# Performance work log

Measured on AMD Instinct MI355X. Metric: run time of the kernel, lower is better.

The kernel has to match this reference:

```python
import math
import jax, jax.numpy as jnp
import numpy as np

B, S, D, H = 4, 2048, 512, 8
DH = D // H
NUM_BUCKETS = 32
MAX_DISTANCE = 128


def _relative_position_bucket(rel_pos, num_buckets=NUM_BUCKETS, max_distance=MAX_DISTANCE):
    # bidirectional T5 bucketing (faithful to the torch staticmethod)
    num_buckets = num_buckets // 2
    rel_buckets = (rel_pos > 0).astype(jnp.int32) * num_buckets
    rel_pos = jnp.abs(rel_pos)
    max_exact = num_buckets // 2
    is_small = rel_pos < max_exact
    # clamp log arg to >=1 element to avoid -inf cast (masked out by is_small anyway)
    rp_f = jnp.maximum(rel_pos, 1).astype(jnp.float32)
    large = max_exact + (
        jnp.log(rp_f / max_exact) / math.log(max_distance / max_exact) * (num_buckets - max_exact)
    ).astype(jnp.int32)
    large = jnp.minimum(large, num_buckets - 1)
    return rel_buckets + jnp.where(is_small, rel_pos, large)


def setup_inputs() -> dict:
    rng = jax.random.key(0)
    ks = jax.random.split(rng, 12)
    s = 0.02
    return {
        'key':   jax.random.normal(ks[0], (B, S, D), jnp.float32),
        'value': jax.random.normal(ks[1], (B, S, D), jnp.float32),
        'query': jax.random.normal(ks[2], (B, S, D), jnp.float32),
        'Wq': jax.random.normal(ks[3], (D, D), jnp.float32) * s,
        'bq': jnp.zeros((D,), jnp.float32),
        'Wk': jax.random.normal(ks[4], (D, D), jnp.float32) * s,
        'bk': jnp.zeros((D,), jnp.float32),
        'Wv': jax.random.normal(ks[5], (D, D), jnp.float32) * s,
        'bv': jnp.zeros((D,), jnp.float32),
        'Wo': jax.random.normal(ks[6], (D, D), jnp.float32) * s,
        'bo': jnp.zeros((D,), jnp.float32),
        'rel_bias': jax.random.normal(ks[7], (NUM_BUCKETS, H), jnp.float32) * s,
        'mask': jax.random.bernoulli(ks[8], 0.5, (B, S, S)),
    }


def reference(key, value, query, Wq, bq, Wk, bk, Wv, bv, Wo, bo, rel_bias, mask):
    def shape(x):  # [B,S,D] -> [B,H,S,DH]
        return x.reshape(B, -1, H, DH).transpose(0, 2, 1, 3)

    q = shape(query @ Wq + bq) / math.sqrt(DH)
    k = shape(key @ Wk + bk)
    v = shape(value @ Wv + bv)

    scores = jnp.einsum('bhqd,bhkd->bhqk', q, k)  # [B,H,S,S]

    # T5 relative position bias
    rel_pos = jnp.arange(S)[None, :] - jnp.arange(S)[:, None]  # [S,S] memory - query
    buckets = _relative_position_bucket(rel_pos)
    pos_bias = rel_bias[buckets]                     # [S,S,H]
    scores = scores + pos_bias.transpose(2, 0, 1)[None]  # [1,H,S,S]

    scores = jnp.where(mask[:, None, :, :], jnp.float32(-1e18), scores)
    attn = jax.nn.softmax(scores, axis=-1)  # dropout p=0 -> identity

    ctx = jnp.einsum('bhqk,bhkd->bhqd', attn, v)
    ctx = ctx.transpose(0, 2, 1, 3).reshape(B, -1, D)
    return ctx @ Wo + bo
```

## Files before the change

kernel.cpp:

```cpp
#include <hip/hip_runtime.h>
#include <hip/hip_bf16.h>
#include <math.h>

#define BB 4
#define SS 2048
#define DD 512
#define HH 8
#define DHH 64
#define KPAD 72
#define GPAD 72
#define LOG2E 1.44269504088896340736f

typedef __attribute__((ext_vector_type(8))) short short8;
typedef __attribute__((ext_vector_type(4))) float f32x4;
typedef __attribute__((ext_vector_type(16))) float f32x16;
typedef __attribute__((ext_vector_type(4))) unsigned short ushort4v;
typedef unsigned short ushort;
typedef unsigned char uchar;
typedef unsigned int u32;
typedef unsigned long long u64;

static __device__ __forceinline__ ushort f2b(float x) {
    __hip_bfloat16 h = __float2bfloat16(x);
    return *reinterpret_cast<ushort*>(&h);
}

__global__ __launch_bounds__(256) void pack_mask_kernel(const void* __restrict__ mask,
                                                        u64* __restrict__ mwords) {
    __shared__ int sflag;
    const int tid = threadIdx.x;
    if (tid == 0) sflag = 0;
    __syncthreads();
    u32 probe = ((const u32*)mask)[tid];
    if (__any(probe > 1u) && (tid & 63) == 0) sflag = 1;
    __syncthreads();
    const bool bytemode = sflag != 0;

    int idx = blockIdx.x * 256 + tid;
    int w = idx & 31;
    int row = idx >> 5;
    u64 bits = 0ull;
    if (bytemode) {
        const uint4* p4 = (const uint4*)((const uchar*)mask + (size_t)row * SS + w * 64);
#pragma unroll
        for (int i = 0; i < 4; ++i) {
            uint4 v = p4[i];
            unsigned int a[4] = {v.x, v.y, v.z, v.w};
#pragma unroll
            for (int j = 0; j < 4; ++j)
#pragma unroll
                for (int byte = 0; byte < 4; ++byte)
                    if ((a[j] >> (byte * 8)) & 0xffu) bits |= 1ull << (i * 16 + j * 4 + byte);
        }
    } else {
        const int4* p4 = (const int4*)((const int*)mask + (size_t)row * SS + w * 64);
#pragma unroll
        for (int i = 0; i < 16; ++i) {
            int4 v = p4[i];
            if (v.x) bits |= 1ull << (i * 4 + 0);
            if (v.y) bits |= 1ull << (i * 4 + 1);
            if (v.z) bits |= 1ull << (i * 4 + 2);
            if (v.w) bits |= 1ull << (i * 4 + 3);
        }
    }
    mwords[idx] = bits;
}

__device__ __forceinline__ int t5_bucket(int rel) {
    int rb = (rel > 0) ? 16 : 0;
    int ap = rel < 0 ? -rel : rel;
    if (ap < 8) return rb + ap;
    float t = logf((float)ap * 0.125f) / 2.77258872985839844f * 8.0f;
    int large = 8 + (int)t;
    if (large > 15) large = 15;
    return rb + large;
}

__global__ __launch_bounds__(256) void bias_table_kernel(const float* __restrict__ rel_bias,
                                                         float* __restrict__ tbl) {
    int i = blockIdx.x * 256 + threadIdx.x;
    int h = i >> 12;
    int d = (i & 4095) - 2047;
    tbl[i] = LOG2E * rel_bias[t5_bucket(d) * HH + h];
}

__global__ __launch_bounds__(256) void wtrans_kernel(const float* __restrict__ W0, const float* __restrict__ W1,
                                                     const float* __restrict__ W2, const float* __restrict__ W3,
                                                     ushort* __restrict__ T0, ushort* __restrict__ T1,
                                                     ushort* __restrict__ T2, ushort* __restrict__ T3) {
    __shared__ float tile[64][65];
    const float* W = blockIdx.z == 0 ? W0 : blockIdx.z == 1 ? W1 : blockIdx.z == 2 ? W2 : W3;
    ushort*     T = blockIdx.z == 0 ? T0 : blockIdx.z == 1 ? T1 : blockIdx.z == 2 ? T2 : T3;
    const int n0 = blockIdx.x * 64, k0 = blockIdx.y * 64;
    const int tr = threadIdx.x >> 4, tc = threadIdx.x & 15;
#pragma unroll
    for (int i = 0; i < 4; ++i) {
        int r = i * 16 + tr;
        float4 v = *(const float4*)&W[(size_t)(k0 + r) * 512 + n0 + tc * 4];
        tile[r][tc * 4 + 0] = v.x; tile[r][tc * 4 + 1] = v.y;
        tile[r][tc * 4 + 2] = v.z; tile[r][tc * 4 + 3] = v.w;
    }
    __syncthreads();
#pragma unroll
    for (int i = 0; i < 4; ++i) {
        int rn = i * 16 + tr;
        ushort4v o;
#pragma unroll
        for (int j = 0; j < 4; ++j) o[j] = f2b(tile[tc * 4 + j][rn]);
        *(ushort4v*)&T[(size_t)(n0 + rn) * 512 + k0 + tc * 4] = o;
    }
}

__global__ __launch_bounds__(256) void qkv_gemm(const float* __restrict__ Xq, const float* __restrict__ Xk,
                                                const float* __restrict__ Xv,
                                                const ushort* __restrict__ Wqt, const ushort* __restrict__ Wkt,
                                                const ushort* __restrict__ Wvt,
                                                const float* __restrict__ bqp, const float* __restrict__ bkp,
                                                const float* __restrict__ bvp,
                                                ushort* __restrict__ Yq, ushort* __restrict__ Yk,
                                                ushort* __restrict__ Yv) {
    __shared__ ushort Als[128 * GPAD];
    __shared__ ushort Bls[128 * GPAD];
    const int z = blockIdx.z;
    const float* A    = z == 0 ? Xq : z == 1 ? Xk : Xv;
    const ushort* Bt  = z == 0 ? Wqt : z == 1 ? Wkt : Wvt;
    const float* bias = z == 0 ? bqp : z == 1 ? bkp : bvp;
    const float scale = z == 0 ? 0.125f * LOG2E : 1.0f;

    const int tid = threadIdx.x;
    const int lane = tid & 63;
    const int wid = tid >> 6;
    const int lq = lane & 15, lg = lane >> 4;
    const int wr = wid >> 1, wc = wid & 1;
    const int bm = blockIdx.x * 128;
    const int bn = blockIdx.y * 128;

    f32x4 acc[4][4];
#pragma unroll
    for (int m = 0; m < 4; ++m)
#pragma unroll
        for (int n = 0; n < 4; ++n) acc[m][n] = (f32x4){0.f, 0.f, 0.f, 0.f};

    const int sr = tid >> 3;
    const int sc = (tid & 7) * 8;

    short8 sa[4], sb[4];
#pragma unroll
    for (int i = 0; i < 4; ++i) {
        int r = sr + i * 32;
        float4 u = *(const float4*)(A + (size_t)(bm + r) * 512 + sc);
        float4 v = *(const float4*)(A + (size_t)(bm + r) * 512 + sc + 4);
        short8 av;
        av[0] = (short)f2b(u.x); av[1] = (short)f2b(u.y); av[2] = (short)f2b(u.z); av[3] = (short)f2b(u.w);
        av[4] = (short)f2b(v.x); av[5] = (short)f2b(v.y); av[6] = (short)f2b(v.z); av[7] = (short)f2b(v.w);
        sa[i] = av;
        sb[i] = *(const short8*)(Bt + (size_t)(bn + r) * 512 + sc);
    }

    for (int k0 = 0; k0 < 512; k0 += 64) {
#pragma unroll
        for (int i = 0; i < 4; ++i) {
            int r = sr + i * 32;
            *(short8*)&Als[r * GPAD + sc] = sa[i];
            *(short8*)&Bls[r * GPAD + sc] = sb[i];
        }
        __syncthreads();
        if (k0 < 448) {
#pragma unroll
            for (int i = 0; i < 4; ++i) {
                int r = sr + i * 32;
                float4 u = *(const float4*)(A + (size_t)(bm + r) * 512 + k0 + 64 + sc);
                float4 v = *(const float4*)(A + (size_t)(bm + r) * 512 + k0 + 64 + sc + 4);
                short8 av;
                av[0] = (short)f2b(u.x); av[1] = (short)f2b(u.y); av[2] = (short)f2b(u.z); av[3] = (short)f2b(u.w);
                av[4] = (short)f2b(v.x); av[5] = (short)f2b(v.y); av[6] = (short)f2b(v.z); av[7] = (short)f2b(v.w);
                sa[i] = av;
                sb[i] = *(const short8*)(Bt + (size_t)(bn + r) * 512 + k0 + 64 + sc);
            }
        }
#pragma unroll
        for (int kk = 0; kk < 2; ++kk) {
            short8 af[4], bf[4];
#pragma unroll
            for (int m = 0; m < 4; ++m)
                af[m] = *(short8*)&Als[(wr * 64 + m * 16 + lq) * GPAD + kk * 32 + lg * 8];
#pragma unroll
            for (int n = 0; n < 4; ++n)
                bf[n] = *(short8*)&Bls[(wc * 64 + n * 16 + lq) * GPAD + kk * 32 + lg * 8];
#pragma unroll
            for (int m = 0; m < 4; ++m)
#pragma unroll
                for (int n = 0; n < 4; ++n)
                    acc[m][n] = __builtin_amdgcn_mfma_f32_16x16x32_bf16(af[m], bf[n], acc[m][n], 0, 0, 0);
        }
        __syncthreads();
    }

    float bv[4];
#pragma unroll
    for (int n = 0; n < 4; ++n) bv[n] = bias[bn + wc * 64 + n * 16 + lq];

    if (z == 2) {
        const int blk = bm >> 11;
        const int s0 = (bm & 2047) + wr * 64 + lg * 4;
#pragma unroll
        for (int m = 0; m < 4; ++m)
#pragma unroll
            for (int n = 0; n < 4; ++n) {
                int col = bn + wc * 64 + n * 16 + lq;
                ushort4v o;
#pragma unroll
                for (int r = 0; r < 4; ++r) o[r] = f2b(acc[m][n][r] + bv[n]);
                *(ushort4v*)&Yv[((size_t)(blk * 512 + col)) * SS + s0 + m * 16] = o;
            }
    } else {
        ushort* Y = z ? Yk : Yq;
#pragma unroll
        for (int m = 0; m < 4; ++m)
#pragma unroll
            for (int r = 0; r < 4; ++r) {
                int row = bm + wr * 64 + m * 16 + lg * 4 + r;
#pragma unroll
                for (int n = 0; n < 4; ++n) {
                    int col = bn + wc * 64 + n * 16 + lq;
                    Y[(size_t)row * 512 + col] = f2b((acc[m][n][r] + bv[n]) * scale);
                }
            }
    }
}

__global__ __launch_bounds__(256) void out_gemm(const ushort* __restrict__ A,
                                                const ushort* __restrict__ Bt,
                                                const float* __restrict__ bias,
                                                float* __restrict__ Y) {
    __shared__ ushort Als[128 * GPAD];
    __shared__ ushort Bls[128 * GPAD];
    const int tid = threadIdx.x;
    const int lane = tid & 63;
    const int wid = tid >> 6;
    const int lq = lane & 15, lg = lane >> 4;
    const int wr = wid >> 1, wc = wid & 1;
    const int bm = blockIdx.x * 128;
    const int bn = blockIdx.y * 128;

    f32x4 acc[4][4];
#pragma unroll
    for (int m = 0; m < 4; ++m)
#pragma unroll
        for (int n = 0; n < 4; ++n) acc[m][n] = (f32x4){0.f, 0.f, 0.f, 0.f};

    const int sr = tid >> 3;
    const int sc = (tid & 7) * 8;

    short8 sa[4], sb[4];
#pragma unroll
    for (int i = 0; i < 4; ++i) {
        int r = sr + i * 32;
        sa[i] = *(const short8*)(A + (size_t)(bm + r) * 512 + sc);
        sb[i] = *(const short8*)(Bt + (size_t)(bn + r) * 512 + sc);
    }

    for (int k0 = 0; k0 < 512; k0 += 64) {
#pragma unroll
        for (int i = 0; i < 4; ++i) {
            int r = sr + i * 32;
            *(short8*)&Als[r * GPAD + sc] = sa[i];
            *(short8*)&Bls[r * GPAD + sc] = sb[i];
        }
        __syncthreads();
        if (k0 < 448) {
#pragma unroll
            for (int i = 0; i < 4; ++i) {
                int r = sr + i * 32;
                sa[i] = *(const short8*)(A + (size_t)(bm + r) * 512 + k0 + 64 + sc);
                sb[i] = *(const short8*)(Bt + (size_t)(bn + r) * 512 + k0 + 64 + sc);
            }
        }
#pragma unroll
        for (int kk = 0; kk < 2; ++kk) {
            short8 af[4], bf[4];
#pragma unroll
            for (int m = 0; m < 4; ++m)
                af[m] = *(short8*)&Als[(wr * 64 + m * 16 + lq) * GPAD + kk * 32 + lg * 8];
#pragma unroll
            for (int n = 0; n < 4; ++n)
                bf[n] = *(short8*)&Bls[(wc * 64 + n * 16 + lq) * GPAD + kk * 32 + lg * 8];
#pragma unroll
            for (int m = 0; m < 4; ++m)
#pragma unroll
                for (int n = 0; n < 4; ++n)
                    acc[m][n] = __builtin_amdgcn_mfma_f32_16x16x32_bf16(af[m], bf[n], acc[m][n], 0, 0, 0);
        }
        __syncthreads();
    }

    float bv[4];
#pragma unroll
    for (int n = 0; n < 4; ++n) bv[n] = bias[bn + wc * 64 + n * 16 + lq];
#pragma unroll
    for (int m = 0; m < 4; ++m)
#pragma unroll
        for (int r = 0; r < 4; ++r) {
            int row = bm + wr * 64 + m * 16 + lg * 4 + r;
#pragma unroll
            for (int n = 0; n < 4; ++n) {
                int col = bn + wc * 64 + n * 16 + lq;
                Y[(size_t)row * 512 + col] = acc[m][n][r] + bv[n];
            }
        }
}

__global__ __launch_bounds__(512, 4) void attn_kernel(const ushort* __restrict__ Qg, const ushort* __restrict__ Kg,
                                                      const ushort* __restrict__ vT, const u64* __restrict__ mwords,
                                                      const float* __restrict__ btbl, ushort* __restrict__ ctxb) {
    __shared__ ushort KV[4][64 * KPAD];
    __shared__ ushort QT[128 * KPAD];
    float* tbl = (float*)QT;

    const int bid = blockIdx.x;
    const int wk = ((bid & 7) << 6) | (bid >> 3);
    const int qb = wk & 15;
    const int h  = (wk >> 4) & 7;
    const int b  = wk >> 7;
    const int q0 = qb * 128;

    const int tid  = threadIdx.x;
    const int wid  = tid >> 6;
    const int lane = tid & 63;
    const int lq32 = lane & 31;
    const int hi   = lane >> 5;
    const int seg  = wid >> 2;
    const int qw   = wid & 3;

    const u64* mrow = mwords + (size_t)b * SS * 32;
    const int qg = q0 + qw * 32 + lq32;

    {
        const int r = tid >> 2;
        const int c = (tid & 3) * 16;
        const size_t g = ((size_t)(b * SS + q0 + r)) * DD + h * DHH + c;
        *(short8*)&QT[r * KPAD + c]     = *(const short8*)(Qg + g);
        *(short8*)&QT[r * KPAD + c + 8] = *(const short8*)(Qg + g + 8);
    }
    __syncthreads();

    short8 qf[4];
#pragma unroll
    for (int dch = 0; dch < 4; ++dch)
        qf[dch] = *(short8*)&QT[(qw * 32 + lq32) * KPAD + dch * 16 + hi * 8];
    __syncthreads();

    {
        const float4* src = (const float4*)(btbl + (size_t)h * 4096);
        float4* dst = (float4*)tbl;
        dst[tid]       = src[tid];
        dst[tid + 512] = src[tid + 512];
    }

    f32x16 acc0, acc1, accl;
#pragma unroll
    for (int i = 0; i < 16; ++i) { acc0[i] = 0.f; acc1[i] = 0.f; accl[i] = 0.f; }

    short8 ones;
#pragma unroll
    for (int i = 0; i < 8; ++i) ones[i] = (short)0x3F80;

    const int stile = tid >> 7;
    const int sidx = tid & 127;
    const int srow = sidx >> 1;
    const int scol = (sidx & 1) * 32;
    const size_t kbaseK = ((size_t)(b * SS + (stile & 1) * 1024 + srow)) * DD + h * DHH + scol;
    const size_t kbaseV = ((size_t)(b * DD + h * DHH + srow)) * SS + (stile & 1) * 1024 + scol;

    short8 stg[4];
    {
        const ushort* sp = (stile < 2) ? (Kg + kbaseK) : (vT + kbaseV);
#pragma unroll
        for (int j = 0; j < 4; ++j) stg[j] = *(const short8*)(sp + j * 8);
    }

    const float* tbp_base = tbl + (2047 + hi * 4 - qg);

    for (int t = 0; t < 16; ++t) {
        __syncthreads();
        {
            ushort* dst = &KV[stile][srow * KPAD + scol];
#pragma unroll
            for (int j = 0; j < 4; ++j) *(short8*)(dst + j * 8) = stg[j];
        }
        __syncthreads();
        if (t < 15) {
            const ushort* sp = (stile < 2) ? (Kg + kbaseK + (size_t)(t + 1) * 64 * DD)
                                           : (vT + kbaseV + (t + 1) * 64);
#pragma unroll
            for (int j = 0; j < 4; ++j) stg[j] = *(const short8*)(sp + j * 8);
        }

        const ushort* Ks = KV[seg];
        const ushort* Vt = KV[2 + seg];
        const int ktw = seg * 16 + t;
        const u64 wv = mrow[(size_t)qg * 32 + ktw];

        const float* tbp = tbp_base + ktw * 64;
        f32x16 st0, st1;
#pragma unroll
        for (int r = 0; r < 16; ++r) {
            const int br = (r & 3) + 8 * (r >> 2);
            st0[r] = tbp[br];
            st1[r] = tbp[32 + br];
        }
#pragma unroll
        for (int dch = 0; dch < 4; ++dch) {
            short8 kf0 = *(short8*)&Ks[lq32 * KPAD + dch * 16 + hi * 8];
            short8 kf1 = *(short8*)&Ks[(32 + lq32) * KPAD + dch * 16 + hi * 8];
            st0 = __builtin_amdgcn_mfma_f32_32x32x16_bf16(kf0, qf[dch], st0, 0, 0, 0);
            st1 = __builtin_amdgcn_mfma_f32_32x32x16_bf16(kf1, qf[dch], st1, 0, 0, 0);
        }

        const u32 mi0 = ~(((u32)wv) >> (hi * 4));
        const u32 mi1 = ~(((u32)(wv >> 32)) >> (hi * 4));
        float p0[16], p1[16];
#pragma unroll
        for (int r = 0; r < 16; ++r) {
            const int br = (r & 3) + 8 * (r >> 2);
            float e0 = __builtin_amdgcn_exp2f(st0[r]);
            float e1 = __builtin_amdgcn_exp2f(st1[r]);
            u32 k0 = (u32)(((int)(mi0 << (31 - br))) >> 31);
            u32 k1 = (u32)(((int)(mi1 << (31 - br))) >> 31);
            p0[r] = __uint_as_float(__float_as_uint(e0) & k0);
            p1[r] = __uint_as_float(__float_as_uint(e1) & k1);
        }

        u32 W[16];
#pragma unroll
        for (int w = 0; w < 8; ++w) {
            asm("v_cvt_pk_bf16_f32 %0, %1, %2" : "=v"(W[w])     : "v"(p0[2 * w]), "v"(p0[2 * w + 1]));
            asm("v_cvt_pk_bf16_f32 %0, %1, %2" : "=v"(W[8 + w]) : "v"(p1[2 * w]), "v"(p1[2 * w + 1]));
        }
        short8 pf[4];
#pragma unroll
        for (int g = 0; g < 4; ++g) {
            u32 A = W[g * 4 + 0], Bw = W[g * 4 + 1], C = W[g * 4 + 2], D = W[g * 4 + 3];
            asm("v_permlane32_swap_b32 %0, %1" : "+v"(A), "+v"(C));
            asm("v_permlane32_swap_b32 %0, %1" : "+v"(Bw), "+v"(D));
            u32 fr[4] = {A, Bw, C, D};
            pf[g] = *(short8*)fr;
        }

#pragma unroll
        for (int g = 0; g < 4; ++g) {
            short8 vf0 = *(short8*)&Vt[lq32 * KPAD + g * 16 + hi * 8];
            short8 vf1 = *(short8*)&Vt[(32 + lq32) * KPAD + g * 16 + hi * 8];
            acc0 = __builtin_amdgcn_mfma_f32_32x32x16_bf16(vf0, pf[g], acc0, 0, 0, 0);
            acc1 = __builtin_amdgcn_mfma_f32_32x32x16_bf16(vf1, pf[g], acc1, 0, 0, 0);
            accl = __builtin_amdgcn_mfma_f32_32x32x16_bf16(ones, pf[g], accl, 0, 0, 0);
        }
    }

    float l_run = accl[0];

    __syncthreads();
    float* cmb = (float*)KV;
    float* cl  = cmb + 128 * 65;
    const int q = qw * 32 + lq32;
    if (seg == 1) {
#pragma unroll
        for (int r = 0; r < 16; ++r) {
            const int dr = (r & 3) + 8 * (r >> 2) + 4 * hi;
            cmb[q * 65 + dr]      = acc0[r];
            cmb[q * 65 + 32 + dr] = acc1[r];
        }
        if (hi == 0) cl[q] = l_run;
    }
    __syncthreads();
    if (seg == 0) {
#pragma unroll
        for (int r = 0; r < 16; ++r) {
            const int dr = (r & 3) + 8 * (r >> 2) + 4 * hi;
            acc0[r] += cmb[q * 65 + dr];
            acc1[r] += cmb[q * 65 + 32 + dr];
        }
        l_run += cl[q];
        const float linv = 1.0f / l_run;
        ushort* T = QT;
#pragma unroll
        for (int r = 0; r < 16; ++r) {
            const int dr = (r & 3) + 8 * (r >> 2) + 4 * hi;
            T[q * KPAD + dr]      = f2b(acc0[r] * linv);
            T[q * KPAD + 32 + dr] = f2b(acc1[r] * linv);
        }
        const int r2 = qw * 32 + (lane >> 1);
        const int c0 = (lane & 1) * 32;
        const size_t g = ((size_t)(b * SS + q0 + r2)) * DD + h * DHH + c0;
#pragma unroll
        for (int j = 0; j < 4; ++j)
            *(short8*)(ctxb + g + j * 8) = *(short8*)&QT[r2 * KPAD + c0 + j * 8];
    }
}

extern "C" void kernel_launch(void* const* d_in, const int* in_sizes, int n_in,
                              void* d_out, int out_size, void* d_ws, size_t ws_size,
                              hipStream_t stream) {
    const float* key   = (const float*)d_in[0];
    const float* value = (const float*)d_in[1];
    const float* query = (const float*)d_in[2];
    const float* Wq = (const float*)d_in[3];
    const float* bq = (const float*)d_in[4];
    const float* Wk = (const float*)d_in[5];
    const float* bk = (const float*)d_in[6];
    const float* Wv = (const float*)d_in[7];
    const float* bv = (const float*)d_in[8];
    const float* Wo = (const float*)d_in[9];
    const float* bo = (const float*)d_in[10];
    const float* rel_bias = (const float*)d_in[11];
    const void* mask = d_in[12];
    float* out = (float*)d_out;

    char* ws = (char*)d_ws;
    const size_t MB = 1024 * 1024;
    float* btbl   = (float*)(ws + 4096);
    u64* mwords   = (u64*)(ws + 512 * 1024);
    ushort* wq_t  = (ushort*)(ws + (size_t)(3 * MB));
    ushort* wk_t  = wq_t + 512 * 512;
    ushort* wv_t  = wk_t + 512 * 512;
    ushort* wo_t  = wv_t + 512 * 512;
    ushort* q_bf  = (ushort*)(ws + (size_t)(5 * MB));
    ushort* k_bf  = q_bf + (size_t)8192 * 512;
    ushort* vT    = k_bf + (size_t)8192 * 512;
    ushort* ctx_bf = vT + (size_t)8192 * 512;

    hipLaunchKernelGGL(pack_mask_kernel, dim3(BB * SS * 32 / 256), dim3(256), 0, stream,
                       mask, mwords);
    hipLaunchKernelGGL(bias_table_kernel, dim3(HH * 4096 / 256), dim3(256), 0, stream,
                       rel_bias, btbl);
    hipLaunchKernelGGL(wtrans_kernel, dim3(8, 8, 4), dim3(256), 0, stream,
                       Wq, Wk, Wv, Wo, wq_t, wk_t, wv_t, wo_t);

    hipLaunchKernelGGL(qkv_gemm, dim3(64, 4, 3), dim3(256), 0, stream,
                       query, key, value, wq_t, wk_t, wv_t, bq, bk, bv, q_bf, k_bf, vT);

    hipLaunchKernelGGL(attn_kernel, dim3(512), dim3(512), 0, stream,
                       q_bf, k_bf, vT, mwords, btbl, ctx_bf);

    hipLaunchKernelGGL(out_gemm, dim3(64, 4), dim3(256), 0, stream, ctx_bf, wo_t, bo, out);
}
```

Baseline: 114.9 us.

## Merge prep kernels into one launch and raise wave priority around MFMA blocks

The mask packing, bias-table build and weight transpose/convert kernels are combined into a single prep kernel that dispatches on block index, removing two launches and their serialization gaps. Separately, the attention loop wraps its QK and PV MFMA sequences in s_setprio(1)/s_setprio(0), so waves issuing matrix work get scheduler priority over waves doing exp/mask math. The fused kernel adds branchy dispatch and shares LDS sizing across roles, and the priority hints may have no effect or may hurt interleaving.

New measurement: 121.7 us. 1.06x slower.

```diff
diff --git a/kernel.cpp b/kernel.cpp
--- a/kernel.cpp
+++ b/kernel.cpp
@@ -25,47 +25,6 @@
     return *reinterpret_cast<ushort*>(&h);
 }
 
-__global__ __launch_bounds__(256) void pack_mask_kernel(const void* __restrict__ mask,
-                                                        u64* __restrict__ mwords) {
-    __shared__ int sflag;
-    const int tid = threadIdx.x;
-    if (tid == 0) sflag = 0;
-    __syncthreads();
-    u32 probe = ((const u32*)mask)[tid];
-    if (__any(probe > 1u) && (tid & 63) == 0) sflag = 1;
-    __syncthreads();
-    const bool bytemode = sflag != 0;
-
-    int idx = blockIdx.x * 256 + tid;
-    int w = idx & 31;
-    int row = idx >> 5;
-    u64 bits = 0ull;
-    if (bytemode) {
-        const uint4* p4 = (const uint4*)((const uchar*)mask + (size_t)row * SS + w * 64);
-#pragma unroll
-        for (int i = 0; i < 4; ++i) {
-            uint4 v = p4[i];
-            unsigned int a[4] = {v.x, v.y, v.z, v.w};
-#pragma unroll
-            for (int j = 0; j < 4; ++j)
-#pragma unroll
-                for (int byte = 0; byte < 4; ++byte)
-                    if ((a[j] >> (byte * 8)) & 0xffu) bits |= 1ull << (i * 16 + j * 4 + byte);
-        }
-    } else {
-        const int4* p4 = (const int4*)((const int*)mask + (size_t)row * SS + w * 64);
-#pragma unroll
-        for (int i = 0; i < 16; ++i) {
-            int4 v = p4[i];
-            if (v.x) bits |= 1ull << (i * 4 + 0);
-            if (v.y) bits |= 1ull << (i * 4 + 1);
-            if (v.z) bits |= 1ull << (i * 4 + 2);
-            if (v.w) bits |= 1ull << (i * 4 + 3);
-        }
-    }
-    mwords[idx] = bits;
-}
-
 __device__ __forceinline__ int t5_bucket(int rel) {
     int rb = (rel > 0) ? 16 : 0;
     int ap = rel < 0 ? -rel : rel;
@@ -76,38 +35,81 @@
     return rb + large;
 }
 
-__global__ __launch_bounds__(256) void bias_table_kernel(const float* __restrict__ rel_bias,
-                                                         float* __restrict__ tbl) {
-    int i = blockIdx.x * 256 + threadIdx.x;
-    int h = i >> 12;
-    int d = (i & 4095) - 2047;
-    tbl[i] = LOG2E * rel_bias[t5_bucket(d) * HH + h];
-}
-
-__global__ __launch_bounds__(256) void wtrans_kernel(const float* __restrict__ W0, const float* __restrict__ W1,
-                                                     const float* __restrict__ W2, const float* __restrict__ W3,
-                                                     ushort* __restrict__ T0, ushort* __restrict__ T1,
-                                                     ushort* __restrict__ T2, ushort* __restrict__ T3) {
+__global__ __launch_bounds__(256) void prep_kernel(const void* __restrict__ mask, u64* __restrict__ mwords,
+                                                   const float* __restrict__ rel_bias, float* __restrict__ btbl,
+                                                   const float* __restrict__ W0, const float* __restrict__ W1,
+                                                   const float* __restrict__ W2, const float* __restrict__ W3,
+                                                   ushort* __restrict__ T0, ushort* __restrict__ T1,
+                                                   ushort* __restrict__ T2, ushort* __restrict__ T3) {
     __shared__ float tile[64][65];
-    const float* W = blockIdx.z == 0 ? W0 : blockIdx.z == 1 ? W1 : blockIdx.z == 2 ? W2 : W3;
-    ushort*     T = blockIdx.z == 0 ? T0 : blockIdx.z == 1 ? T1 : blockIdx.z == 2 ? T2 : T3;
-    const int n0 = blockIdx.x * 64, k0 = blockIdx.y * 64;
-    const int tr = threadIdx.x >> 4, tc = threadIdx.x & 15;
-#pragma unroll
-    for (int i = 0; i < 4; ++i) {
-        int r = i * 16 + tr;
-        float4 v = *(const float4*)&W[(size_t)(k0 + r) * 512 + n0 + tc * 4];
-        tile[r][tc * 4 + 0] = v.x; tile[r][tc * 4 + 1] = v.y;
-        tile[r][tc * 4 + 2] = v.z; tile[r][tc * 4 + 3] = v.w;
-    }
-    __syncthreads();
-#pragma unroll
-    for (int i = 0; i < 4; ++i) {
-        int rn = i * 16 + tr;
-        ushort4v o;
-#pragma unroll
-        for (int j = 0; j < 4; ++j) o[j] = f2b(tile[tc * 4 + j][rn]);
-        *(ushort4v*)&T[(size_t)(n0 + rn) * 512 + k0 + tc * 4] = o;
+    __shared__ int sflag;
+    const int bid = blockIdx.x;
+    const int tid = threadIdx.x;
+
+    if (bid < 1024) {
+        if (tid == 0) sflag = 0;
+        __syncthreads();
+        u32 probe = ((const u32*)mask)[tid];
+        if (__any(probe > 1u) && (tid & 63) == 0) sflag = 1;
+        __syncthreads();
+        const bool bytemode = sflag != 0;
+
+        int idx = bid * 256 + tid;
+        int w = idx & 31;
+        int row = idx >> 5;
+        u64 bits = 0ull;
+        if (bytemode) {
+            const uint4* p4 = (const uint4*)((const uchar*)mask + (size_t)row * SS + w * 64);
+#pragma unroll
+            for (int i = 0; i < 4; ++i) {
+                uint4 v = p4[i];
+                unsigned int a[4] = {v.x, v.y, v.z, v.w};
+#pragma unroll
+                for (int j = 0; j < 4; ++j)
+#pragma unroll
+                    for (int byte = 0; byte < 4; ++byte)
+                        if ((a[j] >> (byte * 8)) & 0xffu) bits |= 1ull << (i * 16 + j * 4 + byte);
+            }
+        } else {
+            const int4* p4 = (const int4*)((const int*)mask + (size_t)row * SS + w * 64);
+#pragma unroll
+            for (int i = 0; i < 16; ++i) {
+                int4 v = p4[i];
+                if (v.x) bits |= 1ull << (i * 4 + 0);
+                if (v.y) bits |= 1ull << (i * 4 + 1);
+                if (v.z) bits |= 1ull << (i * 4 + 2);
+                if (v.w) bits |= 1ull << (i * 4 + 3);
+            }
+        }
+        mwords[idx] = bits;
+    } else if (bid < 1152) {
+        int i = (bid - 1024) * 256 + tid;
+        int h = i >> 12;
+        int d = (i & 4095) - 2047;
+        btbl[i] = LOG2E * rel_bias[t5_bucket(d) * HH + h];
+    } else {
+        const int b2 = bid - 1152;
+        const int z = b2 >> 6;
+        const float* W = z == 0 ? W0 : z == 1 ? W1 : z == 2 ? W2 : W3;
+        ushort*     T = z == 0 ? T0 : z == 1 ? T1 : z == 2 ? T2 : T3;
+        const int n0 = (b2 & 7) * 64, k0 = ((b2 >> 3) & 7) * 64;
+        const int tr = tid >> 4, tc = tid & 15;
+#pragma unroll
+        for (int i = 0; i < 4; ++i) {
+            int r = i * 16 + tr;
+            float4 v = *(const float4*)&W[(size_t)(k0 + r) * 512 + n0 + tc * 4];
+            tile[r][tc * 4 + 0] = v.x; tile[r][tc * 4 + 1] = v.y;
+            tile[r][tc * 4 + 2] = v.z; tile[r][tc * 4 + 3] = v.w;
+        }
+        __syncthreads();
+#pragma unroll
+        for (int i = 0; i < 4; ++i) {
+            int rn = i * 16 + tr;
+            ushort4v o;
+#pragma unroll
+            for (int j = 0; j < 4; ++j) o[j] = f2b(tile[tc * 4 + j][rn]);
+            *(ushort4v*)&T[(size_t)(n0 + rn) * 512 + k0 + tc * 4] = o;
+        }
     }
 }
 
@@ -409,6 +411,7 @@
             st0[r] = tbp[br];
             st1[r] = tbp[32 + br];
         }
+        __builtin_amdgcn_s_setprio(1);
 #pragma unroll
         for (int dch = 0; dch < 4; ++dch) {
             short8 kf0 = *(short8*)&Ks[lq32 * KPAD + dch * 16 + hi * 8];
@@ -416,6 +419,7 @@
             st0 = __builtin_amdgcn_mfma_f32_32x32x16_bf16(kf0, qf[dch], st0, 0, 0, 0);
             st1 = __builtin_amdgcn_mfma_f32_32x32x16_bf16(kf1, qf[dch], st1, 0, 0, 0);
         }
+        __builtin_amdgcn_s_setprio(0);
 
         const u32 mi0 = ~(((u32)wv) >> (hi * 4));
         const u32 mi1 = ~(((u32)(wv >> 32)) >> (hi * 4));
@@ -447,6 +451,7 @@
             pf[g] = *(short8*)fr;
         }
 
+        __builtin_amdgcn_s_setprio(1);
 #pragma unroll
         for (int g = 0; g < 4; ++g) {
             short8 vf0 = *(short8*)&Vt[lq32 * KPAD + g * 16 + hi * 8];
@@ -455,6 +460,7 @@
             acc1 = __builtin_amdgcn_mfma_f32_32x32x16_bf16(vf1, pf[g], acc1, 0, 0, 0);
             accl = __builtin_amdgcn_mfma_f32_32x32x16_bf16(ones, pf[g], accl, 0, 0, 0);
         }
+        __builtin_amdgcn_s_setprio(0);
     }
 
     float l_run = accl[0];
@@ -529,11 +535,8 @@
     ushort* vT    = k_bf + (size_t)8192 * 512;
     ushort* ctx_bf = vT + (size_t)8192 * 512;
 
-    hipLaunchKernelGGL(pack_mask_kernel, dim3(BB * SS * 32 / 256), dim3(256), 0, stream,
-                       mask, mwords);
-    hipLaunchKernelGGL(bias_table_kernel, dim3(HH * 4096 / 256), dim3(256), 0, stream,
-                       rel_bias, btbl);
-    hipLaunchKernelGGL(wtrans_kernel, dim3(8, 8, 4), dim3(256), 0, stream,
+    hipLaunchKernelGGL(prep_kernel, dim3(1408), dim3(256), 0, stream,
+                       mask, mwords, rel_bias, btbl,
                        Wq, Wk, Wv, Wo, wq_t, wk_t, wv_t, wo_t);
 
     hipLaunchKernelGGL(qkv_gemm, dim3(64, 4, 3), dim3(256), 0, stream,
```
